# Kernel tuning notes

Hardware: AMD Instinct MI355X
Metric: run time of the kernel (lower is better)

The kernel has to match this reference:

```python
import jax, jax.numpy as jnp
import numpy as np

IN, HID, OUT = 128, 128, 128
NU, NI = 100000, 50000
E = 500000
NEG_SLOPE = 0.01  # torch F.leaky_relu default


def graph_conv(x_src, W, b, src, dst, n_dst):
    """DGL GraphConv with norm='right': sum messages into dst, divide by in-degree, add bias."""
    h = x_src @ W                                   # [n_src, d_out] -- apply weight first
    agg = jax.ops.segment_sum(h[src], dst, num_segments=n_dst)  # irregular gather + scatter-add
    deg = jax.ops.segment_sum(jnp.ones(dst.shape, h.dtype), dst, num_segments=n_dst)
    return agg / jnp.clip(deg, 1.0)[:, None] + b


def setup_inputs() -> dict:
    key = jax.random.key(0)
    ks = jax.random.split(key, 16)
    inp = {
        "x_user": jax.random.normal(ks[0], (NU, IN), jnp.float32),
        "x_item": jax.random.normal(ks[1], (NI, IN), jnp.float32),
        "src_rates": jax.random.randint(ks[2], (E,), 0, NU),
        "dst_rates": jax.random.randint(ks[3], (E,), 0, NI),
        "src_rev": jax.random.randint(ks[4], (E,), 0, NI),
        "dst_rev": jax.random.randint(ks[5], (E,), 0, NU),
        # layer 1 per-relation GraphConv params
        "W1_rates": jax.random.normal(ks[6], (IN, HID), jnp.float32) / np.sqrt(IN),
        "b1_rates": jnp.zeros((HID,), jnp.float32),
        "W1_rev": jax.random.normal(ks[7], (IN, HID), jnp.float32) / np.sqrt(IN),
        "b1_rev": jnp.zeros((HID,), jnp.float32),
        # layer 2 per-relation GraphConv params
        "W2_rates": jax.random.normal(ks[8], (HID, OUT), jnp.float32) / np.sqrt(HID),
        "b2_rates": jnp.zeros((OUT,), jnp.float32),
        "W2_rev": jax.random.normal(ks[9], (HID, OUT), jnp.float32) / np.sqrt(HID),
        "b2_rev": jnp.zeros((OUT,), jnp.float32),
    }
    return inp


def reference(x_user, x_item, src_rates, dst_rates, src_rev, dst_rev,
              W1_rates, b1_rates, W1_rev, b1_rev,
              W2_rates, b2_rates, W2_rev, b2_rev):
    # layer 1: HeteroGraphConv(sum) -- each dst type receives from its one incoming relation
    h_item = graph_conv(x_user, W1_rates, b1_rates, src_rates, dst_rates, NI)
    h_user = graph_conv(x_item, W1_rev, b1_rev, src_rev, dst_rev, NU)
    h_item = jax.nn.leaky_relu(h_item, NEG_SLOPE)
    h_user = jax.nn.leaky_relu(h_user, NEG_SLOPE)
    # layer 2
    o_item = graph_conv(h_user, W2_rates, b2_rates, src_rates, dst_rates, NI)
    o_user = graph_conv(h_item, W2_rev, b2_rev, src_rev, dst_rev, NU)
    return (o_user, o_item)
```

## Files before the change

### kernel.cpp

```cpp
#include <hip/hip_runtime.h>
#include <cstdint>
#include <cstddef>

#define NUSER 100000
#define NITEM 50000
#define NTOT  150000
#define NEDGE 500000
#define NEG_SLOPE 0.01f
#define PADW 136

#define BROWS 512
#define BSHIFT 9
#define NBUCK ((NTOT + BROWS - 1) / BROWS)
#define GCAP  8192
#define EPB   2048
#define NBINB ((NEDGE + EPB - 1) / EPB)
#define NENT  (2 * EPB)

#define GB_U 352
#define GB_I 176
#define GB1  (GB_U + GB_I)

typedef __attribute__((ext_vector_type(8))) short bf16x8;
typedef __attribute__((ext_vector_type(4))) float f32x4;

__device__ __forceinline__ unsigned short f2bf(float f) {
    unsigned int u = __builtin_bit_cast(unsigned int, f);
    unsigned int r = u + 0x7fffu + ((u >> 16) & 1u);
    return (unsigned short)(r >> 16);
}
__device__ __forceinline__ float bf2f(unsigned int b) {
    unsigned int u = (b & 0xffffu) << 16;
    return __builtin_bit_cast(float, u);
}
__device__ __forceinline__ unsigned int pack2(float lo, float hi) {
    return (unsigned int)f2bf(lo) | ((unsigned int)f2bf(hi) << 16);
}


__global__ __launch_bounds__(512) void bin_wprep(const int* __restrict__ src_rates, const int* __restrict__ dst_rates,
                                                 const int* __restrict__ src_rev,   const int* __restrict__ dst_rev,
                                                 int* __restrict__ bcnt, unsigned int* __restrict__ bbuf,
                                                 const float* __restrict__ w0, const float* __restrict__ w1,
                                                 const float* __restrict__ w2, const float* __restrict__ w3,
                                                 unsigned short* __restrict__ wt) {
    if (blockIdx.x >= NBINB) {
        int widx = blockIdx.x - NBINB;
        const float* src = (widx == 0) ? w0 : (widx == 1) ? w1 : (widx == 2) ? w2 : w3;
        unsigned short* dst = wt + (size_t)widx * 128 * PADW;
        for (int i = threadIdx.x; i < 16384; i += 512) {
            int k = i >> 7, c = i & 127;
            dst[c * PADW + k] = f2bf(src[i]);
        }
        return;
    }

    __shared__ int h[NBUCK];
    __shared__ int hs[NBUCK];
    __shared__ int hbase[NBUCK];
    __shared__ int hcur[NBUCK];
    __shared__ int bsc[512];
    __shared__ unsigned int stage[NENT];

    int t = threadIdx.x;
    int e0 = blockIdx.x * EPB;
    int n = NEDGE - e0; if (n > EPB) n = EPB;

    for (int i = t; i < NBUCK; i += 512) h[i] = 0;
    __syncthreads();

    for (int i = t; i < n; i += 512) {
        int e = e0 + i;
        atomicAdd(&h[dst_rates[e] >> BSHIFT], 1);
        atomicAdd(&h[(NITEM + dst_rev[e]) >> BSHIFT], 1);
    }
    __syncthreads();

    int v = (t < NBUCK) ? h[t] : 0;
    bsc[t] = v;
    __syncthreads();
    for (int off = 1; off < 512; off <<= 1) {
        int x = (t >= off) ? bsc[t - off] : 0;
        __syncthreads();
        bsc[t] += x;
        __syncthreads();
    }
    if (t < NBUCK) {
        int run = bsc[t] - v;
        hs[t] = run;
        hcur[t] = run;
        hbase[t] = (v > 0) ? atomicAdd(&bcnt[t], v) : 0;
    }
    __syncthreads();

    for (int i = t; i < n; i += 512) {
        int e = e0 + i;
        int r1 = dst_rates[e];
        int p1 = atomicAdd(&hcur[r1 >> BSHIFT], 1);
        if (p1 < NENT)
            stage[p1] = ((unsigned)(r1 & (BROWS - 1)) << 17) | (unsigned)src_rates[e];
        int r2 = NITEM + dst_rev[e];
        int p2 = atomicAdd(&hcur[r2 >> BSHIFT], 1);
        if (p2 < NENT)
            stage[p2] = ((unsigned)(r2 & (BROWS - 1)) << 17) | (unsigned)src_rev[e];
    }
    __syncthreads();

    int wid = t >> 6, lane = t & 63;
    for (int b = wid; b < NBUCK; b += 8) {
        int cnt = h[b];
        if (cnt > NENT) cnt = NENT;
        int gb = hbase[b];
        int sb = hs[b];
        for (int i = lane; i < cnt; i += 64) {
            int gpos = gb + i;
            if (gpos < GCAP) bbuf[(size_t)b * GCAP + gpos] = stage[sb + i];
        }
    }
}


struct GemmSm { unsigned short wl[128 * PADW]; unsigned short xl[64 * PADW]; };
struct CsrSm  { unsigned int ent[GCAP]; int h[BROWS]; int hs[BROWS]; int bsc[256]; };
union FusedSm { GemmSm g; CsrSm c; };

__global__ __launch_bounds__(256) void csr_gemm1(const int* __restrict__ bcnt,
                                                 const unsigned int* __restrict__ bbuf,
                                                 int* __restrict__ rp, int* __restrict__ csr,
                                                 const float* __restrict__ xfU, const float* __restrict__ xfI,
                                                 const unsigned short* __restrict__ wt0,
                                                 const unsigned short* __restrict__ wt1,
                                                 unsigned short* __restrict__ outB) {
    __shared__ __attribute__((aligned(16))) FusedSm sm;
    int t = threadIdx.x;
    int bi = blockIdx.x;

    if (bi < GB1) {
        unsigned short* wl = sm.g.wl;
        unsigned short* xl = sm.g.xl;
        bool reg0 = bi < GB_U;
        int tbeg = reg0 ? bi : bi - GB_U;
        int gstr = reg0 ? GB_U : GB_I;
        int rbeg = reg0 ? 0 : NUSER;
        int rcnt = reg0 ? NUSER : NITEM;
        int Nend = rbeg + rcnt;
        int nT = (rcnt + 63) / 64;
        const unsigned short* wt = reg0 ? wt0 : wt1;

        for (int i = t; i < 128 * PADW / 8; i += 256)
            ((uint4*)wl)[i] = ((const uint4*)wt)[i];

        int lane = t & 63, w = t >> 6;
        int l16 = lane & 15, kq = lane >> 4;
        int rowb = w * 16;

        for (int tt = tbeg; tt < nT; tt += gstr) {
            int row0 = rbeg + tt * 64;

            __syncthreads();
            for (int i = t; i < 1024; i += 256) {
                int r = i >> 4, c = i & 15;
                int row = row0 + r;
                uint4 v = make_uint4(0u, 0u, 0u, 0u);
                if (row < Nend) {
                    const float* s = (row < NUSER) ? (xfU + (size_t)row * 128 + c * 8)
                                                   : (xfI + (size_t)(row - NUSER) * 128 + c * 8);
                    float4 a = ((const float4*)s)[0];
                    float4 b = ((const float4*)s)[1];
                    v.x = pack2(a.x, a.y);
                    v.y = pack2(a.z, a.w);
                    v.z = pack2(b.x, b.y);
                    v.w = pack2(b.z, b.w);
                }
                ((uint4*)xl)[r * (PADW / 8) + c] = v;
            }
            __syncthreads();

            f32x4 acc[8];
            #pragma unroll
            for (int i = 0; i < 8; ++i) acc[i] = (f32x4){0.f, 0.f, 0.f, 0.f};

            #pragma unroll
            for (int ks = 0; ks < 4; ++ks) {
                int ko = ks * 32 + kq * 8;
                bf16x8 af = *(const bf16x8*)&xl[(rowb + l16) * PADW + ko];
                #pragma unroll
                for (int t8 = 0; t8 < 8; ++t8) {
                    bf16x8 bf = *(const bf16x8*)&wl[(t8 * 16 + l16) * PADW + ko];
                    acc[t8] = __builtin_amdgcn_mfma_f32_16x16x32_bf16(af, bf, acc[t8], 0, 0, 0);
                }
            }

            #pragma unroll
            for (int t8 = 0; t8 < 8; ++t8) {
                #pragma unroll
                for (int j = 0; j < 4; ++j)
                    xl[(rowb + kq * 4 + j) * PADW + t8 * 16 + l16] = f2bf(acc[t8][j]);
            }
            __syncthreads();
            for (int i = t; i < 1024; i += 256) {
                int r = i >> 4, c = i & 15;
                int row = row0 + r;
                if (row < Nend)
                    ((uint4*)(outB + (size_t)row * 128))[c] = ((uint4*)xl)[r * (PADW / 8) + c];
            }
        }
        return;
    }

    unsigned int* ent = sm.c.ent;
    int* h  = sm.c.h;
    int* hsx = sm.c.hs;
    int* bsc = sm.c.bsc;
    int bk = bi - GB1;

    int ps = 0;
    for (int i = t; i < bk; i += 256) ps += bcnt[i];
    bsc[t] = ps;
    __syncthreads();
    for (int off = 128; off > 0; off >>= 1) {
        if (t < off) bsc[t] += bsc[t + off];
        __syncthreads();
    }
    int base = bsc[0];
    int n = bcnt[bk];
    if (n > GCAP) n = GCAP;
    __syncthreads();

    const unsigned int* src = bbuf + (size_t)bk * GCAP;
    for (int i = t; i < n; i += 256) ent[i] = src[i];
    h[t] = 0; h[t + 256] = 0;
    __syncthreads();

    for (int i = t; i < n; i += 256) atomicAdd(&h[ent[i] >> 17], 1);
    __syncthreads();

    int v0 = h[2 * t], v1 = h[2 * t + 1];
    int ls = v0 + v1;
    bsc[t] = ls;
    __syncthreads();
    for (int off = 1; off < 256; off <<= 1) {
        int x = (t >= off) ? bsc[t - off] : 0;
        __syncthreads();
        bsc[t] += x;
        __syncthreads();
    }
    int run = bsc[t] - ls;
    hsx[2 * t] = run;
    hsx[2 * t + 1] = run + v0;
    __syncthreads();

    for (int r = t; r < BROWS; r += 256) {
        int row = bk * BROWS + r;
        if (row < NTOT) rp[row] = base + hsx[r];
        h[r] = 0;
    }
    if (bk == 0 && t == 0) rp[NTOT] = 2 * NEDGE;
    __syncthreads();

    for (int i = t; i < n; i += 256) {
        unsigned int ev = ent[i];
        int rl = (int)(ev >> 17);
        int pos = base + hsx[rl] + atomicAdd(&h[rl], 1);
        csr[pos] = (int)(ev & 0x1FFFFu);
    }
}


__global__ __launch_bounds__(256) void aggregate_ep(const unsigned short* __restrict__ featA,
                                                    const unsigned short* __restrict__ featB,
                                                    const int* __restrict__ rp, const int* __restrict__ csr,
                                                    const float* __restrict__ bI, const float* __restrict__ bU,
                                                    unsigned short* __restrict__ outb,
                                                    float* __restrict__ outI, float* __restrict__ outU) {
    int row = blockIdx.x * 8 + (threadIdx.x >> 5);
    if (row >= NTOT) return;
    bool item = row < NITEM;
    const unsigned short* feat = item ? featA : featB;
    int l = threadIdx.x & 31;
    int sub = l >> 4, l16 = l & 15;
    int b = rp[row], e = rp[row + 1];
    float a0 = 0.f, a1 = 0.f, a2 = 0.f, a3 = 0.f, a4 = 0.f, a5 = 0.f, a6 = 0.f, a7 = 0.f;
    int j = b + sub;
    for (; j + 2 < e; j += 4) {
        int s0 = csr[j];
        int s1 = csr[j + 2];
        uint4 v0 = *((const uint4*)(feat + (size_t)s0 * 128) + l16);
        uint4 v1 = *((const uint4*)(feat + (size_t)s1 * 128) + l16);
        a0 += bf2f(v0.x); a1 += bf2f(v0.x >> 16);
        a2 += bf2f(v0.y); a3 += bf2f(v0.y >> 16);
        a4 += bf2f(v0.z); a5 += bf2f(v0.z >> 16);
        a6 += bf2f(v0.w); a7 += bf2f(v0.w >> 16);
        a0 += bf2f(v1.x); a1 += bf2f(v1.x >> 16);
        a2 += bf2f(v1.y); a3 += bf2f(v1.y >> 16);
        a4 += bf2f(v1.z); a5 += bf2f(v1.z >> 16);
        a6 += bf2f(v1.w); a7 += bf2f(v1.w >> 16);
    }
    if (j < e) {
        int s0 = csr[j];
        uint4 v0 = *((const uint4*)(feat + (size_t)s0 * 128) + l16);
        a0 += bf2f(v0.x); a1 += bf2f(v0.x >> 16);
        a2 += bf2f(v0.y); a3 += bf2f(v0.y >> 16);
        a4 += bf2f(v0.z); a5 += bf2f(v0.z >> 16);
        a6 += bf2f(v0.w); a7 += bf2f(v0.w >> 16);
    }
    a0 += __shfl_xor(a0, 16); a1 += __shfl_xor(a1, 16);
    a2 += __shfl_xor(a2, 16); a3 += __shfl_xor(a3, 16);
    a4 += __shfl_xor(a4, 16); a5 += __shfl_xor(a5, 16);
    a6 += __shfl_xor(a6, 16); a7 += __shfl_xor(a7, 16);
    if (sub == 0) {
        int deg = e - b;
        float inv = 1.0f / (float)(deg > 0 ? deg : 1);
        const float* bias = item ? bI : bU;
        float4 bv0 = ((const float4*)bias)[l16 * 2];
        float4 bv1 = ((const float4*)bias)[l16 * 2 + 1];
        float r0 = a0 * inv + bv0.x, r1 = a1 * inv + bv0.y;
        float r2 = a2 * inv + bv0.z, r3 = a3 * inv + bv0.w;
        float r4 = a4 * inv + bv1.x, r5 = a5 * inv + bv1.y;
        float r6 = a6 * inv + bv1.z, r7 = a7 * inv + bv1.w;
        if (outI) {
            float* o = item ? (outI + (size_t)row * 128) : (outU + (size_t)(row - NITEM) * 128);
            float4 o0, o1;
            o0.x = r0; o0.y = r1; o0.z = r2; o0.w = r3;
            o1.x = r4; o1.y = r5; o1.z = r6; o1.w = r7;
            ((float4*)o)[l16 * 2]     = o0;
            ((float4*)o)[l16 * 2 + 1] = o1;
        } else {
            r0 = r0 > 0.f ? r0 : NEG_SLOPE * r0;
            r1 = r1 > 0.f ? r1 : NEG_SLOPE * r1;
            r2 = r2 > 0.f ? r2 : NEG_SLOPE * r2;
            r3 = r3 > 0.f ? r3 : NEG_SLOPE * r3;
            r4 = r4 > 0.f ? r4 : NEG_SLOPE * r4;
            r5 = r5 > 0.f ? r5 : NEG_SLOPE * r5;
            r6 = r6 > 0.f ? r6 : NEG_SLOPE * r6;
            r7 = r7 > 0.f ? r7 : NEG_SLOPE * r7;
            uint4 o;
            o.x = pack2(r0, r1);
            o.y = pack2(r2, r3);
            o.z = pack2(r4, r5);
            o.w = pack2(r6, r7);
            *((uint4*)(outb + (size_t)row * 128) + l16) = o;
        }
    }
}


__global__ __launch_bounds__(256) void gemm_both(const unsigned short* __restrict__ inB,
                                                 const unsigned short* __restrict__ wt0,
                                                 const unsigned short* __restrict__ wt1,
                                                 unsigned short* __restrict__ outB,
                                                 int nR0, int g0, int g1) {
    __shared__ __attribute__((aligned(16))) unsigned short wl[128 * PADW];
    __shared__ __attribute__((aligned(16))) unsigned short xl[64 * PADW];
    int t = threadIdx.x;
    int bi = blockIdx.x;
    bool reg0 = bi < g0;
    int tbeg = reg0 ? bi : bi - g0;
    int gstr = reg0 ? g0 : g1;
    int rbeg = reg0 ? 0 : nR0;
    int rcnt = reg0 ? nR0 : NTOT - nR0;
    int Nend = rbeg + rcnt;
    int nT = (rcnt + 63) / 64;
    const unsigned short* wt = reg0 ? wt0 : wt1;

    for (int i = t; i < 128 * PADW / 8; i += 256)
        ((uint4*)wl)[i] = ((const uint4*)wt)[i];

    int lane = t & 63, w = t >> 6;
    int l16 = lane & 15, kq = lane >> 4;
    int rowb = w * 16;

    for (int tt = tbeg; tt < nT; tt += gstr) {
        int row0 = rbeg + tt * 64;

        __syncthreads();
        for (int i = t; i < 1024; i += 256) {
            int r = i >> 4, c = i & 15;
            int row = row0 + r;
            uint4 v = make_uint4(0u, 0u, 0u, 0u);
            if (row < Nend) v = ((const uint4*)(inB + (size_t)row * 128))[c];
            ((uint4*)xl)[r * (PADW / 8) + c] = v;
        }
        __syncthreads();

        f32x4 acc[8];
        #pragma unroll
        for (int i = 0; i < 8; ++i) acc[i] = (f32x4){0.f, 0.f, 0.f, 0.f};

        #pragma unroll
        for (int ks = 0; ks < 4; ++ks) {
            int ko = ks * 32 + kq * 8;
            bf16x8 af = *(const bf16x8*)&xl[(rowb + l16) * PADW + ko];
            #pragma unroll
            for (int t8 = 0; t8 < 8; ++t8) {
                bf16x8 bf = *(const bf16x8*)&wl[(t8 * 16 + l16) * PADW + ko];
                acc[t8] = __builtin_amdgcn_mfma_f32_16x16x32_bf16(af, bf, acc[t8], 0, 0, 0);
            }
        }

        #pragma unroll
        for (int t8 = 0; t8 < 8; ++t8) {
            #pragma unroll
            for (int j = 0; j < 4; ++j)
                xl[(rowb + kq * 4 + j) * PADW + t8 * 16 + l16] = f2bf(acc[t8][j]);
        }
        __syncthreads();
        for (int i = t; i < 1024; i += 256) {
            int r = i >> 4, c = i & 15;
            int row = row0 + r;
            if (row < Nend)
                ((uint4*)(outB + (size_t)row * 128))[c] = ((uint4*)xl)[r * (PADW / 8) + c];
        }
    }
}


extern "C" void kernel_launch(void* const* d_in, const int* in_sizes, int n_in,
                              void* d_out, int out_size, void* d_ws, size_t ws_size,
                              hipStream_t stream) {
    const float* x_user    = (const float*)d_in[0];
    const float* x_item    = (const float*)d_in[1];
    const int*   src_rates = (const int*)d_in[2];
    const int*   dst_rates = (const int*)d_in[3];
    const int*   src_rev   = (const int*)d_in[4];
    const int*   dst_rev   = (const int*)d_in[5];
    const float* W1_rates  = (const float*)d_in[6];
    const float* b1_rates  = (const float*)d_in[7];
    const float* W1_rev    = (const float*)d_in[8];
    const float* b1_rev    = (const float*)d_in[9];
    const float* W2_rates  = (const float*)d_in[10];
    const float* b2_rates  = (const float*)d_in[11];
    const float* W2_rev    = (const float*)d_in[12];
    const float* b2_rev    = (const float*)d_in[13];

    float* out    = (float*)d_out;
    float* o_user = out;
    float* o_item = out + (size_t)NUSER * 128;

    char* ws = (char*)d_ws;
    size_t off = 0;
    auto carve = [&](size_t bytes) -> void* {
        void* p = ws + off;
        off = (off + bytes + 255) & ~(size_t)255;
        return p;
    };
    unsigned short* A = (unsigned short*)carve((size_t)NTOT * 128 * 2);
    unsigned short* B = (unsigned short*)carve((size_t)NTOT * 128 * 2);
    int* rp    = (int*)carve((size_t)(NTOT + 1) * 4);
    int* bcnt  = (int*)carve((size_t)NBUCK * 4);
    int* csr   = (int*)carve((size_t)(2 * NEDGE) * 4);
    unsigned short* wtAll = (unsigned short*)carve((size_t)4 * 128 * PADW * 2);
    unsigned short* Wt1_rates = wtAll;
    unsigned short* Wt1_rev   = wtAll + 1 * (size_t)128 * PADW;
    unsigned short* Wt2_rates = wtAll + 2 * (size_t)128 * PADW;
    unsigned short* Wt2_rev   = wtAll + 3 * (size_t)128 * PADW;

    unsigned int* bbuf = (unsigned int*)B;

    hipMemsetAsync(bcnt, 0, (size_t)NBUCK * 4, stream);
    bin_wprep<<<NBINB + 4, 512, 0, stream>>>(src_rates, dst_rates, src_rev, dst_rev, bcnt, bbuf,
                                             W1_rates, W1_rev, W2_rates, W2_rev, wtAll);

    csr_gemm1<<<GB1 + NBUCK, 256, 0, stream>>>(bcnt, bbuf, rp, csr,
                                               x_user, x_item, Wt1_rates, Wt1_rev, A);

    int nbAgg = (NTOT + 7) / 8;

    aggregate_ep<<<nbAgg, 256, 0, stream>>>(A, A + (size_t)NUSER * 128, rp, csr,
                                            b1_rates, b1_rev, B, nullptr, nullptr);

    gemm_both<<<528, 256, 0, stream>>>(B, Wt2_rev, Wt2_rates, A, NITEM, 176, 352);

    aggregate_ep<<<nbAgg, 256, 0, stream>>>(A + (size_t)NITEM * 128, A, rp, csr,
                                            b2_rates, b2_rev, nullptr, o_item, o_user);
}
```

Measured before the change: 173.1 us.

## Fuse layer-1 aggregation with layer-2 GEMM into one persistent kernel

```diff
diff --git a/kernel.cpp b/kernel.cpp
--- a/kernel.cpp
+++ b/kernel.cpp
@@ -20,6 +20,9 @@
 #define GB_U 352
 #define GB_I 176
 #define GB1  (GB_U + GB_I)
+
+#define AG_I 176
+#define AG_U 352
 
 typedef __attribute__((ext_vector_type(8))) short bf16x8;
 typedef __attribute__((ext_vector_type(4))) float f32x4;
@@ -267,11 +270,142 @@
 }
 
 
+__global__ __launch_bounds__(256) void agg_gemm2(const unsigned short* __restrict__ yU,
+                                                 const unsigned short* __restrict__ yI,
+                                                 const int* __restrict__ rp, const int* __restrict__ csr,
+                                                 const float* __restrict__ b1I, const float* __restrict__ b1U,
+                                                 const unsigned short* __restrict__ wtI,
+                                                 const unsigned short* __restrict__ wtU,
+                                                 unsigned short* __restrict__ outB) {
+    __shared__ __attribute__((aligned(16))) unsigned short wl[128 * PADW];
+    __shared__ __attribute__((aligned(16))) unsigned short xl[64 * PADW];
+    int t = threadIdx.x;
+    int bi = blockIdx.x;
+    bool reg0 = bi < AG_I;
+    int tbeg = reg0 ? bi : bi - AG_I;
+    int gstr = reg0 ? AG_I : AG_U;
+    int rbeg = reg0 ? 0 : NITEM;
+    int rcnt = reg0 ? NITEM : NUSER;
+    int Nend = rbeg + rcnt;
+    int nT = (rcnt + 63) / 64;
+    const unsigned short* feat = reg0 ? yU : yI;
+    const float* bias = reg0 ? b1I : b1U;
+    const unsigned short* wt = reg0 ? wtI : wtU;
+
+    for (int i = t; i < 128 * PADW / 8; i += 256)
+        ((uint4*)wl)[i] = ((const uint4*)wt)[i];
+
+    int hw = t >> 5;
+    int l = t & 31;
+    int sub = l >> 4, l16a = l & 15;
+    int lane = t & 63, w = t >> 6;
+    int l16 = lane & 15, kq = lane >> 4;
+    int rowb = w * 16;
+
+    float4 bv0 = ((const float4*)bias)[l16a * 2];
+    float4 bv1 = ((const float4*)bias)[l16a * 2 + 1];
+
+    for (int tt = tbeg; tt < nT; tt += gstr) {
+        int row0 = rbeg + tt * 64;
+
+        __syncthreads();
+
+        for (int rr = 0; rr < 8; ++rr) {
+            int rl = hw * 8 + rr;
+            int row = row0 + rl;
+            int b = 0, e = 0;
+            if (row < Nend) { b = rp[row]; e = rp[row + 1]; }
+            float a0 = 0.f, a1 = 0.f, a2 = 0.f, a3 = 0.f, a4 = 0.f, a5 = 0.f, a6 = 0.f, a7 = 0.f;
+            int j = b + sub;
+            for (; j + 2 < e; j += 4) {
+                int s0 = csr[j];
+                int s1 = csr[j + 2];
+                uint4 v0 = *((const uint4*)(feat + (size_t)s0 * 128) + l16a);
+                uint4 v1 = *((const uint4*)(feat + (size_t)s1 * 128) + l16a);
+                a0 += bf2f(v0.x); a1 += bf2f(v0.x >> 16);
+                a2 += bf2f(v0.y); a3 += bf2f(v0.y >> 16);
+                a4 += bf2f(v0.z); a5 += bf2f(v0.z >> 16);
+                a6 += bf2f(v0.w); a7 += bf2f(v0.w >> 16);
+                a0 += bf2f(v1.x); a1 += bf2f(v1.x >> 16);
+                a2 += bf2f(v1.y); a3 += bf2f(v1.y >> 16);
+                a4 += bf2f(v1.z); a5 += bf2f(v1.z >> 16);
+                a6 += bf2f(v1.w); a7 += bf2f(v1.w >> 16);
+            }
+            if (j < e) {
+                int s0 = csr[j];
+                uint4 v0 = *((const uint4*)(feat + (size_t)s0 * 128) + l16a);
+                a0 += bf2f(v0.x); a1 += bf2f(v0.x >> 16);
+                a2 += bf2f(v0.y); a3 += bf2f(v0.y >> 16);
+                a4 += bf2f(v0.z); a5 += bf2f(v0.z >> 16);
+                a6 += bf2f(v0.w); a7 += bf2f(v0.w >> 16);
+            }
+            a0 += __shfl_xor(a0, 16); a1 += __shfl_xor(a1, 16);
+            a2 += __shfl_xor(a2, 16); a3 += __shfl_xor(a3, 16);
+            a4 += __shfl_xor(a4, 16); a5 += __shfl_xor(a5, 16);
+            a6 += __shfl_xor(a6, 16); a7 += __shfl_xor(a7, 16);
+            if (sub == 0) {
+                uint4 o = make_uint4(0u, 0u, 0u, 0u);
+                if (row < Nend) {
+                    int deg = e - b;
+                    float inv = 1.0f / (float)(deg > 0 ? deg : 1);
+                    float r0 = a0 * inv + bv0.x, r1 = a1 * inv + bv0.y;
+                    float r2 = a2 * inv + bv0.z, r3 = a3 * inv + bv0.w;
+                    float r4 = a4 * inv + bv1.x, r5 = a5 * inv + bv1.y;
+                    float r6 = a6 * inv + bv1.z, r7 = a7 * inv + bv1.w;
+                    r0 = r0 > 0.f ? r0 : NEG_SLOPE * r0;
+                    r1 = r1 > 0.f ? r1 : NEG_SLOPE * r1;
+                    r2 = r2 > 0.f ? r2 : NEG_SLOPE * r2;
+                    r3 = r3 > 0.f ? r3 : NEG_SLOPE * r3;
+                    r4 = r4 > 0.f ? r4 : NEG_SLOPE * r4;
+                    r5 = r5 > 0.f ? r5 : NEG_SLOPE * r5;
+                    r6 = r6 > 0.f ? r6 : NEG_SLOPE * r6;
+                    r7 = r7 > 0.f ? r7 : NEG_SLOPE * r7;
+                    o.x = pack2(r0, r1);
+                    o.y = pack2(r2, r3);
+                    o.z = pack2(r4, r5);
+                    o.w = pack2(r6, r7);
+                }
+                *((uint4*)(xl + (size_t)rl * PADW) + l16a) = o;
+            }
+        }
+        __syncthreads();
+
+        f32x4 acc[8];
+        #pragma unroll
+        for (int i = 0; i < 8; ++i) acc[i] = (f32x4){0.f, 0.f, 0.f, 0.f};
+
+        #pragma unroll
+        for (int ks = 0; ks < 4; ++ks) {
+            int ko = ks * 32 + kq * 8;
+            bf16x8 af = *(const bf16x8*)&xl[(rowb + l16) * PADW + ko];
+            #pragma unroll
+            for (int t8 = 0; t8 < 8; ++t8) {
+                bf16x8 bf = *(const bf16x8*)&wl[(t8 * 16 + l16) * PADW + ko];
+                acc[t8] = __builtin_amdgcn_mfma_f32_16x16x32_bf16(af, bf, acc[t8], 0, 0, 0);
+            }
+        }
+
+        #pragma unroll
+        for (int t8 = 0; t8 < 8; ++t8) {
+            #pragma unroll
+            for (int j = 0; j < 4; ++j)
+                xl[(rowb + kq * 4 + j) * PADW + t8 * 16 + l16] = f2bf(acc[t8][j]);
+        }
+        __syncthreads();
+        for (int i = t; i < 1024; i += 256) {
+            int r = i >> 4, c = i & 15;
+            int row = row0 + r;
+            if (row < Nend)
+                ((uint4*)(outB + (size_t)row * 128))[c] = ((uint4*)xl)[r * (PADW / 8) + c];
+        }
+    }
+}
+
+
 __global__ __launch_bounds__(256) void aggregate_ep(const unsigned short* __restrict__ featA,
                                                     const unsigned short* __restrict__ featB,
                                                     const int* __restrict__ rp, const int* __restrict__ csr,
                                                     const float* __restrict__ bI, const float* __restrict__ bU,
-                                                    unsigned short* __restrict__ outb,
                                                     float* __restrict__ outI, float* __restrict__ outU) {
     int row = blockIdx.x * 8 + (threadIdx.x >> 5);
     if (row >= NTOT) return;
@@ -314,103 +448,14 @@
         const float* bias = item ? bI : bU;
         float4 bv0 = ((const float4*)bias)[l16 * 2];
         float4 bv1 = ((const float4*)bias)[l16 * 2 + 1];
-        float r0 = a0 * inv + bv0.x, r1 = a1 * inv + bv0.y;
-        float r2 = a2 * inv + bv0.z, r3 = a3 * inv + bv0.w;
-        float r4 = a4 * inv + bv1.x, r5 = a5 * inv + bv1.y;
-        float r6 = a6 * inv + bv1.z, r7 = a7 * inv + bv1.w;
-        if (outI) {
-            float* o = item ? (outI + (size_t)row * 128) : (outU + (size_t)(row - NITEM) * 128);
-            float4 o0, o1;
-            o0.x = r0; o0.y = r1; o0.z = r2; o0.w = r3;
-            o1.x = r4; o1.y = r5; o1.z = r6; o1.w = r7;
-            ((float4*)o)[l16 * 2]     = o0;
-            ((float4*)o)[l16 * 2 + 1] = o1;
-        } else {
-            r0 = r0 > 0.f ? r0 : NEG_SLOPE * r0;
-            r1 = r1 > 0.f ? r1 : NEG_SLOPE * r1;
-            r2 = r2 > 0.f ? r2 : NEG_SLOPE * r2;
-            r3 = r3 > 0.f ? r3 : NEG_SLOPE * r3;
-            r4 = r4 > 0.f ? r4 : NEG_SLOPE * r4;
-            r5 = r5 > 0.f ? r5 : NEG_SLOPE * r5;
-            r6 = r6 > 0.f ? r6 : NEG_SLOPE * r6;
-            r7 = r7 > 0.f ? r7 : NEG_SLOPE * r7;
-            uint4 o;
-            o.x = pack2(r0, r1);
-            o.y = pack2(r2, r3);
-            o.z = pack2(r4, r5);
-            o.w = pack2(r6, r7);
-            *((uint4*)(outb + (size_t)row * 128) + l16) = o;
-        }
-    }
-}
-
-
-__global__ __launch_bounds__(256) void gemm_both(const unsigned short* __restrict__ inB,
-                                                 const unsigned short* __restrict__ wt0,
-                                                 const unsigned short* __restrict__ wt1,
-                                                 unsigned short* __restrict__ outB,
-                                                 int nR0, int g0, int g1) {
-    __shared__ __attribute__((aligned(16))) unsigned short wl[128 * PADW];
-    __shared__ __attribute__((aligned(16))) unsigned short xl[64 * PADW];
-    int t = threadIdx.x;
-    int bi = blockIdx.x;
-    bool reg0 = bi < g0;
-    int tbeg = reg0 ? bi : bi - g0;
-    int gstr = reg0 ? g0 : g1;
-    int rbeg = reg0 ? 0 : nR0;
-    int rcnt = reg0 ? nR0 : NTOT - nR0;
-    int Nend = rbeg + rcnt;
-    int nT = (rcnt + 63) / 64;
-    const unsigned short* wt = reg0 ? wt0 : wt1;
-
-    for (int i = t; i < 128 * PADW / 8; i += 256)
-        ((uint4*)wl)[i] = ((const uint4*)wt)[i];
-
-    int lane = t & 63, w = t >> 6;
-    int l16 = lane & 15, kq = lane >> 4;
-    int rowb = w * 16;
-
-    for (int tt = tbeg; tt < nT; tt += gstr) {
-        int row0 = rbeg + tt * 64;
-
-        __syncthreads();
-        for (int i = t; i < 1024; i += 256) {
-            int r = i >> 4, c = i & 15;
-            int row = row0 + r;
-            uint4 v = make_uint4(0u, 0u, 0u, 0u);
-            if (row < Nend) v = ((const uint4*)(inB + (size_t)row * 128))[c];
-            ((uint4*)xl)[r * (PADW / 8) + c] = v;
-        }
-        __syncthreads();
-
-        f32x4 acc[8];
-        #pragma unroll
-        for (int i = 0; i < 8; ++i) acc[i] = (f32x4){0.f, 0.f, 0.f, 0.f};
-
-        #pragma unroll
-        for (int ks = 0; ks < 4; ++ks) {
-            int ko = ks * 32 + kq * 8;
-            bf16x8 af = *(const bf16x8*)&xl[(rowb + l16) * PADW + ko];
-            #pragma unroll
-            for (int t8 = 0; t8 < 8; ++t8) {
-                bf16x8 bf = *(const bf16x8*)&wl[(t8 * 16 + l16) * PADW + ko];
-                acc[t8] = __builtin_amdgcn_mfma_f32_16x16x32_bf16(af, bf, acc[t8], 0, 0, 0);
-            }
-        }
-
-        #pragma unroll
-        for (int t8 = 0; t8 < 8; ++t8) {
-            #pragma unroll
-            for (int j = 0; j < 4; ++j)
-                xl[(rowb + kq * 4 + j) * PADW + t8 * 16 + l16] = f2bf(acc[t8][j]);
-        }
-        __syncthreads();
-        for (int i = t; i < 1024; i += 256) {
-            int r = i >> 4, c = i & 15;
-            int row = row0 + r;
-            if (row < Nend)
-                ((uint4*)(outB + (size_t)row * 128))[c] = ((uint4*)xl)[r * (PADW / 8) + c];
-        }
+        float* o = item ? (outI + (size_t)row * 128) : (outU + (size_t)(row - NITEM) * 128);
+        float4 o0, o1;
+        o0.x = a0 * inv + bv0.x; o0.y = a1 * inv + bv0.y;
+        o0.z = a2 * inv + bv0.z; o0.w = a3 * inv + bv0.w;
+        o1.x = a4 * inv + bv1.x; o1.y = a5 * inv + bv1.y;
+        o1.z = a6 * inv + bv1.z; o1.w = a7 * inv + bv1.w;
+        ((float4*)o)[l16 * 2]     = o0;
+        ((float4*)o)[l16 * 2 + 1] = o1;
     }
 }
 
@@ -464,13 +509,10 @@
     csr_gemm1<<<GB1 + NBUCK, 256, 0, stream>>>(bcnt, bbuf, rp, csr,
                                                x_user, x_item, Wt1_rates, Wt1_rev, A);
 
+    agg_gemm2<<<AG_I + AG_U, 256, 0, stream>>>(A, A + (size_t)NUSER * 128, rp, csr,
+                                               b1_rates, b1_rev, Wt2_rev, Wt2_rates, B);
+
     int nbAgg = (NTOT + 7) / 8;
-
-    aggregate_ep<<<nbAgg, 256, 0, stream>>>(A, A + (size_t)NUSER * 128, rp, csr,
-                                            b1_rates, b1_rev, B, nullptr, nullptr);
-
-    gemm_both<<<528, 256, 0, stream>>>(B, Wt2_rev, Wt2_rates, A, NITEM, 176, 352);
-
-    aggregate_ep<<<nbAgg, 256, 0, stream>>>(A + (size_t)NITEM * 128, A, rp, csr,
-                                            b2_rates, b2_rev, nullptr, o_item, o_user);
-}
+    aggregate_ep<<<nbAgg, 256, 0, stream>>>(B + (size_t)NITEM * 128, B, rp, csr,
+                                            b2_rates, b2_rev, o_item, o_user);
+}
```

Result: slower. 239.9 us (+38.5%).
